# Optimization experiments

Hardware: AMD Instinct MI355X
Metric: run time of the kernel (lower is better)

The kernel has to match this reference:

```python
import jax, jax.numpy as jnp
import numpy as np


def _trilinear_sample(src, iz, iy, ix):
    """grid_sample 3D, mode='bilinear' (trilinear), padding_mode='zeros', on unnormalized voxel coords.
    src: [B,C,D,H,W]; iz,iy,ix: [B,D,H,W] float voxel coords (iz indexes D, iy H, ix W)."""
    B, C, D, H, W = src.shape
    z0 = jnp.floor(iz); y0 = jnp.floor(iy); x0 = jnp.floor(ix)
    tz = iz - z0; ty = iy - y0; tx = ix - x0
    z0i = z0.astype(jnp.int32); y0i = y0.astype(jnp.int32); x0i = x0.astype(jnp.int32)
    src_flat = src.reshape(B, C, D * H * W)

    def corner(dz, dy, dx):
        zc = z0i + dz; yc = y0i + dy; xc = x0i + dx
        valid = (zc >= 0) & (zc < D) & (yc >= 0) & (yc < H) & (xc >= 0) & (xc < W)
        zcc = jnp.clip(zc, 0, D - 1); ycc = jnp.clip(yc, 0, H - 1); xcc = jnp.clip(xc, 0, W - 1)
        lin = (zcc * H + ycc) * W + xcc                      # [B,D,H,W] flat spatial index
        vals = jax.vmap(lambda v, i: v[:, i.ravel()])(src_flat, lin)  # [B,C,D*H*W]
        vals = vals.reshape(B, C, D, H, W)
        wz = tz if dz else (1.0 - tz)
        wy = ty if dy else (1.0 - ty)
        wx = tx if dx else (1.0 - tx)
        w = (wz * wy * wx) * valid.astype(src.dtype)         # zeros padding
        return vals * w[:, None]

    out = jnp.zeros_like(src)
    for dz in (0, 1):
        for dy in (0, 1):
            for dx in (0, 1):
                out = out + corner(dz, dy, dx)
    return out


def reference(src, flow):
    B, _, D, H, W = flow.shape
    dt = flow.dtype
    # identity grid, channels ordered (z,y,x) i.e. (D,H,W), matching torch.meshgrid indexing='ij'
    gz, gy, gx = jnp.meshgrid(jnp.arange(D, dtype=dt), jnp.arange(H, dtype=dt),
                              jnp.arange(W, dtype=dt), indexing='ij')
    grid = jnp.stack([gz, gy, gx])[None]                     # [1,3,D,H,W]
    coords = grid + flow                                      # absolute voxel coords
    denom = jnp.array([D - 1, H - 1, W - 1], dtype=dt).reshape(1, 3, 1, 1, 1)
    norm = 2.0 * (coords / denom - 0.5)                       # normalized to [-1,1]
    # grid_sample expects last-dim order (x,y,z); align_corners=True unnormalization:
    ix = (norm[:, 2] + 1.0) * (W - 1) * 0.5
    iy = (norm[:, 1] + 1.0) * (H - 1) * 0.5
    iz = (norm[:, 0] + 1.0) * (D - 1) * 0.5
    return _trilinear_sample(src, iz, iy, ix)


def setup_inputs() -> dict:
    key = jax.random.key(0)
    k1, k2 = jax.random.split(key)
    B, C, D, H, W = 2, 2, 128, 160, 128
    src = jax.random.normal(k1, (B, C, D, H, W), dtype=jnp.float32)
    flow = jax.random.normal(k2, (B, 3, D, H, W), dtype=jnp.float32)
    return {"src": src, "flow": flow}
```

## Files before the change

kernel.cpp:

```cpp
#include <hip/hip_runtime.h>


#define B_ 2
#define C_ 2
#define D_ 128
#define H_ 160
#define W_ 128
constexpr int S_ = D_ * H_ * W_;

#define ZT 8
#define YT 8
#define XT 32
#define RZ 3
#define RY 3
#define RX 4
#define CZ (ZT + 2 * RZ)
#define CY (YT + 2 * RY)
#define CX (XT + 2 * RX)
#define NTHREADS 512
#define PLANE_PAD 8192

typedef const __attribute__((address_space(1))) unsigned int ga_u32;
typedef __attribute__((address_space(3))) unsigned int lds_u32;

__device__ __forceinline__ void gload16(const float* g, float* l) {
    __builtin_amdgcn_global_load_lds((ga_u32*)g, (lds_u32*)l, 16, 0, 0);
}

struct PState {
    int o00, o01, o10, o11;
    float w00, w01, w10, w11, wx0, wx1;
    bool hi0, lo1, fast;
};

__device__ __forceinline__ PState mk_state(
    int x, int y, int z, float fz, float fy, float fx,
    int zb, int yb, int xb,
    int zlo, int zhi, int ylo, int yhi, int xlo, int xhi)
{
    const float iz = (float)z + fz;
    const float iy = (float)y + fy;
    const float ix = (float)x + fx;

    const float zf = floorf(iz), yf = floorf(iy), xf = floorf(ix);
    const float tz = iz - zf, ty = iy - yf, tx = ix - xf;
    const int z0 = (int)zf, y0 = (int)yf, x0 = (int)xf;

    const int zc0 = min(max(z0, 0), D_ - 1), zc1 = min(max(z0 + 1, 0), D_ - 1);
    const int yc0 = min(max(y0, 0), H_ - 1), yc1 = min(max(y0 + 1, 0), H_ - 1);
    const int xp  = min(max(x0, 0), W_ - 2);

    const float wz0 = ((unsigned)z0       < (unsigned)D_) ? (1.f - tz) : 0.f;
    const float wz1 = ((unsigned)(z0 + 1) < (unsigned)D_) ? tz         : 0.f;
    const float wy0 = ((unsigned)y0       < (unsigned)H_) ? (1.f - ty) : 0.f;
    const float wy1 = ((unsigned)(y0 + 1) < (unsigned)H_) ? ty         : 0.f;

    PState st;
    st.wx0 = ((unsigned)x0       < (unsigned)W_) ? (1.f - tx) : 0.f;
    st.wx1 = ((unsigned)(x0 + 1) < (unsigned)W_) ? tx         : 0.f;
    st.hi0 = x0 > xp;
    st.lo1 = x0 < xp;
    st.w00 = wz0 * wy0; st.w01 = wz0 * wy1;
    st.w10 = wz1 * wy0; st.w11 = wz1 * wy1;
    st.fast = (zc0 >= zlo) & (zc1 < zhi) &
              (yc0 >= ylo) & (yc1 < yhi) &
              (xp >= xlo) & (xp + 1 < xhi);
    if (st.fast) {
        const int izl0 = zc0 - (zb - RZ), izl1 = zc1 - (zb - RZ);
        const int iyl0 = yc0 - (yb - RY), iyl1 = yc1 - (yb - RY);
        const int ixl  = xp - (xb - RX);
        st.o00 = (izl0 * CY + iyl0) * CX + ixl;
        st.o01 = (izl0 * CY + iyl1) * CX + ixl;
        st.o10 = (izl1 * CY + iyl0) * CX + ixl;
        st.o11 = (izl1 * CY + iyl1) * CX + ixl;
    } else {
        st.o00 = (zc0 * H_ + yc0) * W_ + xp;
        st.o01 = (zc0 * H_ + yc1) * W_ + xp;
        st.o10 = (zc1 * H_ + yc0) * W_ + xp;
        st.o11 = (zc1 * H_ + yc1) * W_ + xp;
    }
    return st;
}

__device__ __forceinline__ float eval_ch(const PState& st,
                                         const float* __restrict__ ldsp,
                                         const float* __restrict__ gp)
{
    float a00, b00, a01, b01, a10, b10, a11, b11;
    if (st.fast) {
        a00 = ldsp[st.o00]; b00 = ldsp[st.o00 + 1];
        a01 = ldsp[st.o01]; b01 = ldsp[st.o01 + 1];
        a10 = ldsp[st.o10]; b10 = ldsp[st.o10 + 1];
        a11 = ldsp[st.o11]; b11 = ldsp[st.o11 + 1];
    } else {
        a00 = gp[st.o00]; b00 = gp[st.o00 + 1];
        a01 = gp[st.o01]; b01 = gp[st.o01 + 1];
        a10 = gp[st.o10]; b10 = gp[st.o10 + 1];
        a11 = gp[st.o11]; b11 = gp[st.o11 + 1];
    }
    const float q00 = st.wx0 * (st.hi0 ? b00 : a00) + st.wx1 * (st.lo1 ? a00 : b00);
    const float q01 = st.wx0 * (st.hi0 ? b01 : a01) + st.wx1 * (st.lo1 ? a01 : b01);
    const float q10 = st.wx0 * (st.hi0 ? b10 : a10) + st.wx1 * (st.lo1 ? a10 : b10);
    const float q11 = st.wx0 * (st.hi0 ? b11 : a11) + st.wx1 * (st.lo1 ? a11 : b11);
    return st.w00 * q00 + st.w01 * q01 + st.w10 * q10 + st.w11 * q11;
}

__global__ __launch_bounds__(NTHREADS, 4) void warp3d_tile(
    const float* __restrict__ src,
    const float* __restrict__ flow,
    float* __restrict__ out)
{
    __shared__ float tile[2 * PLANE_PAD];

    const int tid = threadIdx.x;
    const int xb = blockIdx.x * XT;
    const int yb = blockIdx.y * YT;
    const int bz = blockIdx.z;
    const int zb = (bz & 15) * ZT;
    const int b  = bz >> 4;

    const float* fb = flow + (long long)b * 3 * S_;
    const float* s0 = src + (long long)b * C_ * S_;
    float* o0       = out + (long long)b * C_ * S_;

#pragma unroll
    for (int j = 0; j < 4; ++j) {
        const int lin = j * NTHREADS + tid;
        const int row = lin / 10;
        const int cq  = lin - row * 10;
        const int rz = row / CY, ry = row - rz * CY;
        const int gz = min(max(zb - RZ + rz, 0), D_ - 1);
        const int gy = min(max(yb - RY + ry, 0), H_ - 1);
        const int gx = min(max(xb - RX + cq * 4, 0), W_ - 4);
        gload16(s0 + (gz * H_ + gy) * W_ + gx, &tile[lin * 4]);
    }

    const int xq = tid & 7;
    const int ly = (tid >> 3) & 7;
    const int lz = tid >> 6;
    const int x0g = xb + xq * 4;
    const int y = yb + ly, z = zb + lz;
    const int sbase = (z * H_ + y) * W_ + x0g;
    const float4 fz4 = *(const float4*)(fb + sbase);
    const float4 fy4 = *(const float4*)(fb + S_ + sbase);
    const float4 fx4 = *(const float4*)(fb + 2 * S_ + sbase);

    __builtin_amdgcn_sched_barrier(0);

#pragma unroll
    for (int j = 0; j < 4; ++j) {
        const int lin = j * NTHREADS + tid;
        const int row = lin / 10;
        const int cq  = lin - row * 10;
        const int rz = row / CY, ry = row - rz * CY;
        const int gz = min(max(zb - RZ + rz, 0), D_ - 1);
        const int gy = min(max(yb - RY + ry, 0), H_ - 1);
        const int gx = min(max(xb - RX + cq * 4, 0), W_ - 4);
        gload16(s0 + S_ + (gz * H_ + gy) * W_ + gx, &tile[PLANE_PAD + lin * 4]);
    }

    __builtin_amdgcn_sched_barrier(0);

    asm volatile("s_waitcnt vmcnt(4)" ::: "memory");
    __builtin_amdgcn_sched_barrier(0);
    __builtin_amdgcn_s_barrier();
    __builtin_amdgcn_sched_barrier(0);

    const int zlo = max(0, zb - RZ), zhi = min(D_, zb + ZT + RZ);
    const int ylo = max(0, yb - RY), yhi = min(H_, yb + YT + RY);
    const int xlo = max(0, xb - RX), xhi = min(W_, xb + XT + RX);

    const PState st0 = mk_state(x0g + 0, y, z, fz4.x, fy4.x, fx4.x,
                                zb, yb, xb, zlo, zhi, ylo, yhi, xlo, xhi);
    const PState st1 = mk_state(x0g + 1, y, z, fz4.y, fy4.y, fx4.y,
                                zb, yb, xb, zlo, zhi, ylo, yhi, xlo, xhi);
    const PState st2 = mk_state(x0g + 2, y, z, fz4.z, fy4.z, fx4.z,
                                zb, yb, xb, zlo, zhi, ylo, yhi, xlo, xhi);
    const PState st3 = mk_state(x0g + 3, y, z, fz4.w, fy4.w, fx4.w,
                                zb, yb, xb, zlo, zhi, ylo, yhi, xlo, xhi);

    const float c0a = eval_ch(st0, tile, s0);
    const float c0b = eval_ch(st1, tile, s0);
    const float c0c = eval_ch(st2, tile, s0);
    const float c0d = eval_ch(st3, tile, s0);

    asm volatile("s_waitcnt vmcnt(0)" ::: "memory");
    __builtin_amdgcn_sched_barrier(0);
    *(float4*)(o0 + sbase) = make_float4(c0a, c0b, c0c, c0d);
    __builtin_amdgcn_s_barrier();
    __builtin_amdgcn_sched_barrier(0);

    const float c1a = eval_ch(st0, tile + PLANE_PAD, s0 + S_);
    const float c1b = eval_ch(st1, tile + PLANE_PAD, s0 + S_);
    const float c1c = eval_ch(st2, tile + PLANE_PAD, s0 + S_);
    const float c1d = eval_ch(st3, tile + PLANE_PAD, s0 + S_);

    *(float4*)(o0 + S_ + sbase) = make_float4(c1a, c1b, c1c, c1d);
}

extern "C" void kernel_launch(void* const* d_in, const int* in_sizes, int n_in,
                              void* d_out, int out_size, void* d_ws, size_t ws_size,
                              hipStream_t stream) {
    const float* src  = (const float*)d_in[0];
    const float* flow = (const float*)d_in[1];
    float* out = (float*)d_out;

    dim3 grid(W_ / XT, H_ / YT, (D_ / ZT) * B_);
    warp3d_tile<<<grid, NTHREADS, 0, stream>>>(src, flow, out);
}
```

Measured before the change: 189.1 us.

## March blocks along z with double-buffered LDS halo tiles and prefetched flow

Each block becomes persistent over a 64-deep z chunk and walks it in 8 steps. The next step's halo tile and flow values are prefetched into a second LDS buffer while the current step is evaluated. The y tile size changes to 10, and both channels are staged in one pass. Fallback global gathers are issued before the wait, so their latency overlaps the async loads. This amortizes launch and halo overhead and hides load latency, at the cost of lower occupancy (launch bounds 2), about 147KB of dynamic LDS, and only 256 blocks in total.

```diff
diff --git a/kernel.cpp b/kernel.cpp
--- a/kernel.cpp
+++ b/kernel.cpp
@@ -9,7 +9,7 @@
 constexpr int S_ = D_ * H_ * W_;
 
 #define ZT 8
-#define YT 8
+#define YT 10
 #define XT 32
 #define RZ 3
 #define RY 3
@@ -18,13 +18,41 @@
 #define CY (YT + 2 * RY)
 #define CX (XT + 2 * RX)
 #define NTHREADS 512
-#define PLANE_PAD 8192
+#define PLANE (CZ * CY * CX)
+#define CHPP (PLANE / 4)
+#define NCHUNK (2 * CHPP)
+#define NPAD (9 * NTHREADS)
+#define BUFFL (NPAD * 4)
+#define ZCHUNK 64
+#define NSTEP 8
+#define ZSTRIDE (ZT * H_ * W_)
+#define PAIRS 5
 
 typedef const __attribute__((address_space(1))) unsigned int ga_u32;
 typedef __attribute__((address_space(3))) unsigned int lds_u32;
 
 __device__ __forceinline__ void gload16(const float* g, float* l) {
     __builtin_amdgcn_global_load_lds((ga_u32*)g, (lds_u32*)l, 16, 0, 0);
+}
+
+__device__ __forceinline__ void stage_tile(const float* __restrict__ s0,
+                                           float* __restrict__ buf,
+                                           int zb, int yb, int xb, int tid)
+{
+#pragma unroll
+    for (int j = 0; j < 9; ++j) {
+        const int lin = j * NTHREADS + tid;
+        const int r   = (lin < NCHUNK) ? lin : (lin - NCHUNK);
+        const int pl  = (r >= CHPP) ? 1 : 0;
+        const int rem = r - pl * CHPP;
+        const int row = rem / 10;
+        const int cq  = rem - row * 10;
+        const int rz = row >> 4, ry = row & 15;
+        const int gz = min(max(zb - RZ + rz, 0), D_ - 1);
+        const int gy = min(max(yb - RY + ry, 0), H_ - 1);
+        const int gx = min(max(xb - RX + cq * 4, 0), W_ - 4);
+        gload16(s0 + pl * S_ + (gz * H_ + gy) * W_ + gx, &buf[lin * 4]);
+    }
 }
 
 struct PState {
@@ -82,22 +110,12 @@
     return st;
 }
 
-__device__ __forceinline__ float eval_ch(const PState& st,
-                                         const float* __restrict__ ldsp,
-                                         const float* __restrict__ gp)
-{
-    float a00, b00, a01, b01, a10, b10, a11, b11;
-    if (st.fast) {
-        a00 = ldsp[st.o00]; b00 = ldsp[st.o00 + 1];
-        a01 = ldsp[st.o01]; b01 = ldsp[st.o01 + 1];
-        a10 = ldsp[st.o10]; b10 = ldsp[st.o10 + 1];
-        a11 = ldsp[st.o11]; b11 = ldsp[st.o11 + 1];
-    } else {
-        a00 = gp[st.o00]; b00 = gp[st.o00 + 1];
-        a01 = gp[st.o01]; b01 = gp[st.o01 + 1];
-        a10 = gp[st.o10]; b10 = gp[st.o10 + 1];
-        a11 = gp[st.o11]; b11 = gp[st.o11 + 1];
-    }
+__device__ __forceinline__ float eval_any(const PState& st, const float* p)
+{
+    const float a00 = p[st.o00], b00 = p[st.o00 + 1];
+    const float a01 = p[st.o01], b01 = p[st.o01 + 1];
+    const float a10 = p[st.o10], b10 = p[st.o10 + 1];
+    const float a11 = p[st.o11], b11 = p[st.o11 + 1];
     const float q00 = st.wx0 * (st.hi0 ? b00 : a00) + st.wx1 * (st.lo1 ? a00 : b00);
     const float q01 = st.wx0 * (st.hi0 ? b01 : a01) + st.wx1 * (st.lo1 ? a01 : b01);
     const float q10 = st.wx0 * (st.hi0 ? b10 : a10) + st.wx1 * (st.lo1 ? a10 : b10);
@@ -105,97 +123,111 @@
     return st.w00 * q00 + st.w01 * q01 + st.w10 * q10 + st.w11 * q11;
 }
 
-__global__ __launch_bounds__(NTHREADS, 4) void warp3d_tile(
+__global__ __launch_bounds__(NTHREADS, 2) void warp3d_march(
     const float* __restrict__ src,
     const float* __restrict__ flow,
     float* __restrict__ out)
 {
-    __shared__ float tile[2 * PLANE_PAD];
+    extern __shared__ float tile[];
 
     const int tid = threadIdx.x;
     const int xb = blockIdx.x * XT;
     const int yb = blockIdx.y * YT;
     const int bz = blockIdx.z;
-    const int zb = (bz & 15) * ZT;
-    const int b  = bz >> 4;
+    const int zc = (bz & 1) * ZCHUNK;
+    const int b  = bz >> 1;
 
     const float* fb = flow + (long long)b * 3 * S_;
     const float* s0 = src + (long long)b * C_ * S_;
     float* o0       = out + (long long)b * C_ * S_;
 
-#pragma unroll
-    for (int j = 0; j < 4; ++j) {
-        const int lin = j * NTHREADS + tid;
-        const int row = lin / 10;
-        const int cq  = lin - row * 10;
-        const int rz = row / CY, ry = row - rz * CY;
-        const int gz = min(max(zb - RZ + rz, 0), D_ - 1);
-        const int gy = min(max(yb - RY + ry, 0), H_ - 1);
-        const int gx = min(max(xb - RX + cq * 4, 0), W_ - 4);
-        gload16(s0 + (gz * H_ + gy) * W_ + gx, &tile[lin * 4]);
-    }
-
-    const int xq = tid & 7;
-    const int ly = (tid >> 3) & 7;
-    const int lz = tid >> 6;
-    const int x0g = xb + xq * 4;
-    const int y = yb + ly, z = zb + lz;
-    const int sbase = (z * H_ + y) * W_ + x0g;
-    const float4 fz4 = *(const float4*)(fb + sbase);
-    const float4 fy4 = *(const float4*)(fb + S_ + sbase);
-    const float4 fx4 = *(const float4*)(fb + 2 * S_ + sbase);
-
-    __builtin_amdgcn_sched_barrier(0);
-
-#pragma unroll
-    for (int j = 0; j < 4; ++j) {
-        const int lin = j * NTHREADS + tid;
-        const int row = lin / 10;
-        const int cq  = lin - row * 10;
-        const int rz = row / CY, ry = row - rz * CY;
-        const int gz = min(max(zb - RZ + rz, 0), D_ - 1);
-        const int gy = min(max(yb - RY + ry, 0), H_ - 1);
-        const int gx = min(max(xb - RX + cq * 4, 0), W_ - 4);
-        gload16(s0 + S_ + (gz * H_ + gy) * W_ + gx, &tile[PLANE_PAD + lin * 4]);
-    }
-
-    __builtin_amdgcn_sched_barrier(0);
-
-    asm volatile("s_waitcnt vmcnt(4)" ::: "memory");
-    __builtin_amdgcn_sched_barrier(0);
-    __builtin_amdgcn_s_barrier();
-    __builtin_amdgcn_sched_barrier(0);
-
-    const int zlo = max(0, zb - RZ), zhi = min(D_, zb + ZT + RZ);
+    int lxk[PAIRS], lyk[PAIRS], lzk[PAIRS], sk[PAIRS];
+#pragma unroll
+    for (int k = 0; k < PAIRS; ++k) {
+        const int vox = k * NTHREADS + tid;
+        lxk[k] = vox & 31;
+        const int r = vox >> 5;
+        lyk[k] = r % 10;
+        lzk[k] = r / 10;
+        sk[k] = ((zc + lzk[k]) * H_ + yb + lyk[k]) * W_ + xb + lxk[k];
+    }
+
     const int ylo = max(0, yb - RY), yhi = min(H_, yb + YT + RY);
     const int xlo = max(0, xb - RX), xhi = min(W_, xb + XT + RX);
 
-    const PState st0 = mk_state(x0g + 0, y, z, fz4.x, fy4.x, fx4.x,
-                                zb, yb, xb, zlo, zhi, ylo, yhi, xlo, xhi);
-    const PState st1 = mk_state(x0g + 1, y, z, fz4.y, fy4.y, fx4.y,
-                                zb, yb, xb, zlo, zhi, ylo, yhi, xlo, xhi);
-    const PState st2 = mk_state(x0g + 2, y, z, fz4.z, fy4.z, fx4.z,
-                                zb, yb, xb, zlo, zhi, ylo, yhi, xlo, xhi);
-    const PState st3 = mk_state(x0g + 3, y, z, fz4.w, fy4.w, fx4.w,
-                                zb, yb, xb, zlo, zhi, ylo, yhi, xlo, xhi);
-
-    const float c0a = eval_ch(st0, tile, s0);
-    const float c0b = eval_ch(st1, tile, s0);
-    const float c0c = eval_ch(st2, tile, s0);
-    const float c0d = eval_ch(st3, tile, s0);
-
-    asm volatile("s_waitcnt vmcnt(0)" ::: "memory");
-    __builtin_amdgcn_sched_barrier(0);
-    *(float4*)(o0 + sbase) = make_float4(c0a, c0b, c0c, c0d);
-    __builtin_amdgcn_s_barrier();
-    __builtin_amdgcn_sched_barrier(0);
-
-    const float c1a = eval_ch(st0, tile + PLANE_PAD, s0 + S_);
-    const float c1b = eval_ch(st1, tile + PLANE_PAD, s0 + S_);
-    const float c1c = eval_ch(st2, tile + PLANE_PAD, s0 + S_);
-    const float c1d = eval_ch(st3, tile + PLANE_PAD, s0 + S_);
-
-    *(float4*)(o0 + S_ + sbase) = make_float4(c1a, c1b, c1c, c1d);
+    stage_tile(s0, tile, zc, yb, xb, tid);
+    float fzc[PAIRS], fyc[PAIRS], fxc[PAIRS];
+#pragma unroll
+    for (int k = 0; k < PAIRS; ++k) {
+        fzc[k] = fb[sk[k]];
+        fyc[k] = fb[S_ + sk[k]];
+        fxc[k] = fb[2 * S_ + sk[k]];
+    }
+
+#pragma unroll 1
+    for (int t = 0; t < NSTEP; ++t) {
+        __builtin_amdgcn_sched_barrier(0);
+        const int zb = zc + t * ZT;
+        const bool more = (t + 1 < NSTEP);
+        const float* bufc = tile + (t & 1) * BUFFL;
+        float* bufn       = tile + ((t + 1) & 1) * BUFFL;
+        const int zlo = max(0, zb - RZ), zhi = min(D_, zb + ZT + RZ);
+
+        PState st[PAIRS];
+        float a0[PAIRS], a1[PAIRS];
+#pragma unroll
+        for (int k = 0; k < PAIRS; ++k)
+            st[k] = mk_state(xb + lxk[k], yb + lyk[k], zb + lzk[k],
+                             fzc[k], fyc[k], fxc[k],
+                             zb, yb, xb, zlo, zhi, ylo, yhi, xlo, xhi);
+
+#pragma unroll
+        for (int k = 0; k < PAIRS; ++k)
+            if (!st[k].fast) {
+                a0[k] = eval_any(st[k], s0);
+                a1[k] = eval_any(st[k], s0 + S_);
+            }
+        __builtin_amdgcn_sched_barrier(0);
+
+        if (more) stage_tile(s0, bufn, zb + ZT, yb, xb, tid);
+        float fzn[PAIRS], fyn[PAIRS], fxn[PAIRS];
+        int sn[PAIRS];
+#pragma unroll
+        for (int k = 0; k < PAIRS; ++k) {
+            sn[k] = sk[k] + (more ? ZSTRIDE : 0);
+            fzn[k] = fb[sn[k]];
+            fyn[k] = fb[S_ + sn[k]];
+            fxn[k] = fb[2 * S_ + sn[k]];
+        }
+        __builtin_amdgcn_sched_barrier(0);
+
+        if (more) { asm volatile("s_waitcnt vmcnt(24)" ::: "memory"); }
+        else      { asm volatile("s_waitcnt vmcnt(15)" ::: "memory"); }
+        __builtin_amdgcn_sched_barrier(0);
+        __builtin_amdgcn_s_barrier();
+        __builtin_amdgcn_sched_barrier(0);
+
+#pragma unroll
+        for (int k = 0; k < PAIRS; ++k)
+            if (st[k].fast) {
+                a0[k] = eval_any(st[k], bufc);
+                a1[k] = eval_any(st[k], bufc + PLANE);
+            }
+
+#pragma unroll
+        for (int k = 0; k < PAIRS; ++k) {
+            o0[sk[k]]      = a0[k];
+            o0[S_ + sk[k]] = a1[k];
+        }
+
+        __builtin_amdgcn_s_barrier();
+        __builtin_amdgcn_sched_barrier(0);
+
+#pragma unroll
+        for (int k = 0; k < PAIRS; ++k) {
+            fzc[k] = fzn[k]; fyc[k] = fyn[k]; fxc[k] = fxn[k]; sk[k] = sn[k];
+        }
+    }
 }
 
 extern "C" void kernel_launch(void* const* d_in, const int* in_sizes, int n_in,
@@ -205,6 +237,14 @@
     const float* flow = (const float*)d_in[1];
     float* out = (float*)d_out;
 
-    dim3 grid(W_ / XT, H_ / YT, (D_ / ZT) * B_);
-    warp3d_tile<<<grid, NTHREADS, 0, stream>>>(src, flow, out);
-}
+    static bool attr_set = false;
+    if (!attr_set) {
+        hipFuncSetAttribute(reinterpret_cast<const void*>(warp3d_march),
+                            hipFuncAttributeMaxDynamicSharedMemorySize,
+                            2 * BUFFL * (int)sizeof(float));
+        attr_set = true;
+    }
+
+    dim3 grid(W_ / XT, H_ / YT, (D_ / ZCHUNK) * B_);
+    warp3d_march<<<grid, NTHREADS, 2 * BUFFL * sizeof(float), stream>>>(src, flow, out);
+}
```

After: 164.6 us. -12.9%, faster.
